# Kernel tuning notes

Measured on AMD Instinct MI355X. Metric: run time of the kernel, lower is better.

Reference implementation:

```python
import jax, jax.numpy as jnp
import numpy as np


def _lstm(x, Wx, Wh, b):
    """Fused-gate LSTM over time axis 1. x: [B,T,I]; Wx: [I,4H]; Wh: [H,4H]; b: [4H].
    Gate order (i, f, g, o) as in flax.linen.LSTMCell. Zero initial carry."""
    B, T, _ = x.shape
    H = Wh.shape[0]
    # Precompute all input-to-gate contributions in one big GEMM.
    xg = jnp.einsum('bti,ih->bth', x, Wx) + b  # [B,T,4H]

    def step(carry, xt):
        c, h = carry
        z = xt + h @ Wh  # [B,4H]
        i, f, g, o = jnp.split(z, 4, axis=-1)
        c = jax.nn.sigmoid(f) * c + jax.nn.sigmoid(i) * jnp.tanh(g)
        h = jax.nn.sigmoid(o) * jnp.tanh(c)
        return (c, h), h

    init = (jnp.zeros((B, H), x.dtype), jnp.zeros((B, H), x.dtype))
    _, hs = jax.lax.scan(step, init, jnp.swapaxes(xg, 0, 1))  # hs: [T,B,H]
    return jnp.swapaxes(hs, 0, 1)  # [B,T,H]


def _forward(X, conv_w, conv_b,
             Wx1, Wh1, b1, Wx2, Wh2, b2, Wx3, Wh3, b3, Wx4, Wh4, b4,
             Wa, ba, Va, bva, Wd1, bd1, Wd2, bd2):
    # 1-D conv, SAME padding (flax default), NWC layout.
    x = jax.lax.conv_general_dilated(X, conv_w, (1,), 'SAME',
                                     dimension_numbers=('NWC', 'WIO', 'NWC')) + conv_b
    # NOTE: source uses jnp.flip(..., axis=-1) -> flips FEATURE axis (faithful to source).
    x1 = _lstm(x, Wx1, Wh1, b1)
    x2 = _lstm(jnp.flip(x, axis=-1), Wx2, Wh2, b2)
    x = jnp.concatenate([x1, x2], axis=-1)  # [B,T,2F]
    x1 = _lstm(x, Wx3, Wh3, b3)
    x2 = _lstm(jnp.flip(x, axis=-1), Wx4, Wh4, b4)
    enc = jnp.concatenate([x1, x2], axis=-1)  # [B,T,4F]
    # Additive attention: softmax over time axis.
    score = jnp.tanh(enc @ Wa + ba) @ Va + bva  # [B,T,1]
    w = jax.nn.softmax(score, axis=1)
    ctx = jnp.sum(w * enc, axis=1)  # [B,4F]
    # MLP head (dropout deterministic -> identity).
    h = jnp.tanh(ctx @ Wd1 + bd1)
    return h @ Wd2 + bd2  # [B,1]


def setup_inputs() -> dict:
    key = jax.random.key(0)
    B, T, Cin, F = 32, 4096, 8, 64
    ks = iter(jax.random.split(key, 32))

    def w(shape):
        fan_in = shape[0] if len(shape) <= 2 else shape[0] * shape[1]
        return jax.random.normal(next(ks), shape, jnp.float32) / np.sqrt(fan_in)

    d = {}
    d['X'] = jax.random.normal(next(ks), (B, T, Cin), jnp.float32)
    d['conv_w'] = w((4, Cin, 16))
    d['conv_b'] = jnp.zeros((16,), jnp.float32)
    lstm_dims = {'1': (16, F), '2': (16, F), '3': (2 * F, 2 * F), '4': (2 * F, 2 * F)}
    for n, (i_dim, h_dim) in lstm_dims.items():
        d['Wx' + n] = w((i_dim, 4 * h_dim))
        d['Wh' + n] = w((h_dim, 4 * h_dim))
        d['b' + n] = jnp.zeros((4 * h_dim,), jnp.float32)
    d['Wa'] = w((4 * F, F)); d['ba'] = jnp.zeros((F,), jnp.float32)
    d['Va'] = w((F, 1));     d['bva'] = jnp.zeros((1,), jnp.float32)
    d['Wd1'] = w((4 * F, F)); d['bd1'] = jnp.zeros((F,), jnp.float32)
    d['Wd2'] = w((F, 1));     d['bd2'] = jnp.zeros((1,), jnp.float32)
    d['deterministic'] = 1
    return d


def reference(X, conv_w, conv_b,
              Wx1, Wh1, b1, Wx2, Wh2, b2, Wx3, Wh3, b3, Wx4, Wh4, b4,
              Wa, ba, Va, bva, Wd1, bd1, Wd2, bd2, deterministic):
    # deterministic=1 -> dropout is the identity; already reflected in _forward.
    return _forward(X, conv_w, conv_b,
                    Wx1, Wh1, b1, Wx2, Wh2, b2, Wx3, Wh3, b3, Wx4, Wh4, b4,
                    Wa, ba, Va, bva, Wd1, bd1, Wd2, bd2)
```

## Files before the change

### kernel.cpp

```cpp
#include <hip/hip_runtime.h>


#define TFULL 4096
#define NB 32

__device__ __forceinline__ float fexp2(float x){ return __builtin_amdgcn_exp2f(x); }
__device__ __forceinline__ float frcp(float x){ return __builtin_amdgcn_rcpf(x); }
__device__ __forceinline__ float sigf(float x){ return frcp(1.f + fexp2(-1.44269504f*x)); }
__device__ __forceinline__ float tanh_(float x){
    float e = fexp2(fminf(2.88539008f*x, 126.f));
    return (e - 1.f) * frcp(e + 1.f);
}
#define PIN4(v) asm volatile("" : "+v"(v.x), "+v"(v.y), "+v"(v.z), "+v"(v.w))

__global__ __launch_bounds__(256) void k_init(float* __restrict__ st1,
        float* __restrict__ st2, float* __restrict__ am, float* __restrict__ al,
        float* __restrict__ acc){
    int i = blockIdx.x * 256 + threadIdx.x;
    if (i < 8192)  st1[i] = 0.f;
    if (i < 16384) st2[i] = 0.f;
    if (i < 8192)  acc[i] = 0.f;
    if (i < 32){ am[i] = -3.4e38f; al[i] = 0.f; }
}

__global__ __launch_bounds__(256) void k_pack(
        const float* __restrict__ Wx1, const float* __restrict__ Wh1, const float* __restrict__ b1,
        const float* __restrict__ Wx2, const float* __restrict__ Wh2, const float* __restrict__ b2,
        const float* __restrict__ Wx3, const float* __restrict__ Wh3, const float* __restrict__ b3,
        const float* __restrict__ Wx4, const float* __restrict__ Wh4, const float* __restrict__ b4,
        float* __restrict__ W34, float* __restrict__ b34, float* __restrict__ W2p,
        float* __restrict__ W1p, float* __restrict__ b12){
    int i0 = blockIdx.x * 256 + threadIdx.x;
    int stride = gridDim.x * 256;
    for (int e = i0; e < 131072; e += stride){
        int k = e >> 10, n = e & 1023;
        W34[e] = (n < 512) ? Wx3[k*512 + n] : Wx4[(127 - k)*512 + (n - 512)];
    }
    for (int e = i0; e < 1024; e += stride) b34[e] = (e < 512) ? b3[e] : b4[e - 512];
    for (int e = i0; e < 131072; e += stride){
        int l = e >> 16, r = e & 65535, tid = r >> 6, widx = r & 63;
        int q = tid & 127, s = tid >> 7;
        int m = widx >> 4, kk = widx & 15;
        W2p[e] = (l ? Wh4 : Wh3)[(16*s + kk)*512 + 4*q + m];
    }
    for (int e = i0; e < 65536; e += stride){
        int l = e >> 15, r = e & 32767, tid = r >> 6, wq = r & 63;
        int q = tid & 63, s = tid >> 6;
        float v = 0.f;
        if (wq < 32){
            int c = wq >> 3, k = wq & 7;
            v = (l ? Wh2 : Wh1)[(s*8 + k)*256 + (4*q + c)];
        } else if (s < 2){
            int c = (wq - 32) >> 3, rr = (wq - 32) & 7;
            int rg = s*8 + rr, col = 4*q + c;
            v = l ? Wx2[(15 - rg)*256 + col] : Wx1[rg*256 + col];
        }
        W1p[e] = v;
    }
    for (int e = i0; e < 512; e += stride) b12[e] = (e < 256) ? b1[e] : b2[e - 256];
}

__global__ __launch_bounds__(256) void k_conv(const float* __restrict__ X,
        const float* __restrict__ W, const float* __restrict__ Bv,
        float* __restrict__ out, int t0, int lc){
    __shared__ float Ws[512];
    __shared__ float bs[16];
    int tid = threadIdx.x;
    Ws[tid] = W[tid]; Ws[tid + 256] = W[tid + 256];
    if (tid < 16) bs[tid] = Bv[tid];
    __syncthreads();
    int m = blockIdx.x * 256 + tid;
    int b = m >> lc, trel = m & ((1 << lc) - 1);
    int t = t0 + trel;
    float o[16];
    #pragma unroll
    for (int co = 0; co < 16; ++co) o[co] = bs[co];
    #pragma unroll
    for (int w = 0; w < 4; ++w){
        int tt = t + w - 1;
        if (tt >= 0 && tt < TFULL){
            const float* xr = X + ((size_t)(b << 12) + tt) * 8;
            #pragma unroll
            for (int ci = 0; ci < 8; ++ci){
                float v = xr[ci];
                #pragma unroll
                for (int co = 0; co < 16; ++co) o[co] += v * Ws[(w*8 + ci)*16 + co];
            }
        }
    }
    float* op = out + (size_t)m * 16;
    #pragma unroll
    for (int q = 0; q < 4; ++q)
        *(float4*)(op + q*4) = make_float4(o[q*4], o[q*4+1], o[q*4+2], o[q*4+3]);
}

__global__ void __launch_bounds__(512, 2)
k_scan1(const float* __restrict__ x, const float* __restrict__ W1p,
        const float* __restrict__ b12,
        float* __restrict__ cc, float* __restrict__ st1, int C){
    int l = blockIdx.x >> 5;
    int b = blockIdx.x & 31;
    int tid = threadIdx.x;
    int q = tid & 63;
    int s = tid >> 6;
    float4 w[16];
    {
        const float4* wp = (const float4*)(W1p + ((size_t)l*512 + tid)*64);
        #pragma unroll
        for (int i = 0; i < 16; ++i) w[i] = wp[i];
        #pragma unroll
        for (int i = 0; i < 16; ++i) PIN4(w[i]);
    }
    float bval = (tid < 256) ? b12[l*256 + tid] : 0.f;

    __shared__ float xs[128 * 16];
    __shared__ float zp[8 * 256];
    __shared__ float actb[256];
    __shared__ float ccbuf[128 * 64];
    __shared__ float hbufs[64];
    float c = 0.f;
    int sidx = (l*32 + b)*64 + q;
    if (tid < 64){ c = st1[sidx]; hbufs[tid] = st1[4096 + sidx]; }
    __syncthreads();

    const float* xb = x + ((size_t)b * C) * 16;
    float* ccb = cc + ((size_t)b * C) * 128 + (l << 6);
    int BS = C < 128 ? C : 128;
    int bsm = BS - 1;
    int fr = tid >> 2, fi = tid & 3;

    #pragma clang loop unroll(disable)
    for (int t = 0; t < C; ++t){
        int st = t & bsm;
        if (st == 0){
            __syncthreads();
            if (t && fr < BS){
                const float4* cb4 = (const float4*)ccbuf + fr*16 + fi*4;
                float4* cgp = (float4*)(ccb + (size_t)(t - BS + fr)*128) + fi*4;
                #pragma unroll
                for (int i = 0; i < 4; ++i) cgp[i] = cb4[i];
            }
            if (tid < BS*4)
                ((float4*)xs)[tid] = ((const float4*)(xb + (size_t)t*16))[tid];
            __syncthreads();
        }
        float a0 = 0.f, a1 = 0.f, a2 = 0.f, a3 = 0.f;
        const float4* hb4 = (const float4*)hbufs + (s << 1);
        #pragma unroll
        for (int k4 = 0; k4 < 2; ++k4){
            float4 hv = hb4[k4];
            a0 = fmaf(hv.x, w[k4].x, a0);     a0 = fmaf(hv.y, w[k4].y, a0);
            a0 = fmaf(hv.z, w[k4].z, a0);     a0 = fmaf(hv.w, w[k4].w, a0);
            a1 = fmaf(hv.x, w[2+k4].x, a1);   a1 = fmaf(hv.y, w[2+k4].y, a1);
            a1 = fmaf(hv.z, w[2+k4].z, a1);   a1 = fmaf(hv.w, w[2+k4].w, a1);
            a2 = fmaf(hv.x, w[4+k4].x, a2);   a2 = fmaf(hv.y, w[4+k4].y, a2);
            a2 = fmaf(hv.z, w[4+k4].z, a2);   a2 = fmaf(hv.w, w[4+k4].w, a2);
            a3 = fmaf(hv.x, w[6+k4].x, a3);   a3 = fmaf(hv.y, w[6+k4].y, a3);
            a3 = fmaf(hv.z, w[6+k4].z, a3);   a3 = fmaf(hv.w, w[6+k4].w, a3);
        }
        if (s < 2){
            const float4* xr = (const float4*)(xs + st * 16) + (s << 1);
            #pragma unroll
            for (int r4 = 0; r4 < 2; ++r4){
                float4 xv = xr[r4];
                a0 = fmaf(xv.x, w[8+r4].x, a0);    a0 = fmaf(xv.y, w[8+r4].y, a0);
                a0 = fmaf(xv.z, w[8+r4].z, a0);    a0 = fmaf(xv.w, w[8+r4].w, a0);
                a1 = fmaf(xv.x, w[10+r4].x, a1);   a1 = fmaf(xv.y, w[10+r4].y, a1);
                a1 = fmaf(xv.z, w[10+r4].z, a1);   a1 = fmaf(xv.w, w[10+r4].w, a1);
                a2 = fmaf(xv.x, w[12+r4].x, a2);   a2 = fmaf(xv.y, w[12+r4].y, a2);
                a2 = fmaf(xv.z, w[12+r4].z, a2);   a2 = fmaf(xv.w, w[12+r4].w, a2);
                a3 = fmaf(xv.x, w[14+r4].x, a3);   a3 = fmaf(xv.y, w[14+r4].y, a3);
                a3 = fmaf(xv.z, w[14+r4].z, a3);   a3 = fmaf(xv.w, w[14+r4].w, a3);
            }
        }
        *(float4*)(zp + (s << 8) + (q << 2)) = make_float4(a0, a1, a2, a3);
        __syncthreads();
        if (tid < 256){
            float z = bval;
            #pragma unroll
            for (int ss = 0; ss < 8; ++ss) z += zp[(ss << 8) + tid];
            actb[tid] = (tid >> 6) == 2 ? tanh_(z) : sigf(z);
        }
        __syncthreads();
        if (tid < 64){
            float gi = actb[tid], gf = actb[64 + tid];
            float gg = actb[128 + tid], go = actb[192 + tid];
            c = gf * c + gi * gg;
            float h = go * tanh_(c);
            hbufs[tid] = h;
            ccbuf[st*64 + tid] = h;
        }
        __syncthreads();
    }
    if (fr < BS){
        const float4* cb4 = (const float4*)ccbuf + fr*16 + fi*4;
        float4* cgp = (float4*)(ccb + (size_t)(C - BS + fr)*128) + fi*4;
        #pragma unroll
        for (int i = 0; i < 4; ++i) cgp[i] = cb4[i];
    }
    if (tid < 64){ st1[sidx] = c; st1[4096 + sidx] = hbufs[tid]; }
}

template<bool TANH>
__global__ __launch_bounds__(128) void k_gemm(
        const float* __restrict__ A, int lda,
        const float* __restrict__ B, int ldb,
        const float* __restrict__ bias,
        float* __restrict__ Cm, int ldc, int K){
    __shared__ float As[64 * 129];
    __shared__ float Bs[64 * 68];
    int tid = threadIdx.x;
    int tx = tid & 7;
    int ty = tid >> 3;
    int r0 = blockIdx.x * 128;
    int n0 = blockIdx.y * 64;
    float acc[8][8];
    #pragma unroll
    for (int i = 0; i < 8; ++i)
        #pragma unroll
        for (int n = 0; n < 8; ++n) acc[i][n] = 0.f;

    for (int kb = 0; kb < K; kb += 64){
        __syncthreads();
        for (int idx = tid; idx < 2048; idx += 128){
            int r = idx >> 4, k4 = idx & 15;
            float4 v = *(const float4*)(A + (size_t)(r0 + r) * lda + kb + k4*4);
            As[(k4*4 + 0)*129 + r] = v.x;
            As[(k4*4 + 1)*129 + r] = v.y;
            As[(k4*4 + 2)*129 + r] = v.z;
            As[(k4*4 + 3)*129 + r] = v.w;
        }
        for (int idx = tid; idx < 1024; idx += 128){
            int n4 = idx & 15, k = idx >> 4;
            float4 v = *(const float4*)(B + (size_t)(kb + k) * ldb + n0 + n4*4);
            *(float4*)(Bs + k*68 + n4*4) = v;
        }
        __syncthreads();
        #pragma unroll 4
        for (int k = 0; k < 64; ++k){
            float a[8];
            #pragma unroll
            for (int i = 0; i < 8; ++i) a[i] = As[k*129 + ty*8 + i];
            float4 b0 = *(const float4*)(Bs + k*68 + tx*8);
            float4 b1 = *(const float4*)(Bs + k*68 + tx*8 + 4);
            float bq[8] = {b0.x, b0.y, b0.z, b0.w, b1.x, b1.y, b1.z, b1.w};
            #pragma unroll
            for (int i = 0; i < 8; ++i)
                #pragma unroll
                for (int n = 0; n < 8; ++n) acc[i][n] += a[i] * bq[n];
        }
    }
    #pragma unroll
    for (int i = 0; i < 8; ++i){
        size_t rr = (size_t)r0 + ty*8 + i;
        float* cp = Cm + rr * ldc + n0 + tx*8;
        float ov[8];
        #pragma unroll
        for (int n = 0; n < 8; ++n){
            float v = acc[i][n] + bias[n0 + tx*8 + n];
            ov[n] = TANH ? tanh_(v) : v;
        }
        *(float4*)cp       = make_float4(ov[0], ov[1], ov[2], ov[3]);
        *(float4*)(cp + 4) = make_float4(ov[4], ov[5], ov[6], ov[7]);
    }
}

__global__ void __launch_bounds__(1024, 4)
k_scan2(const float* __restrict__ xg, const float* __restrict__ W2p,
        float* __restrict__ enc, float* __restrict__ st2, int C){
    int l = blockIdx.x >> 5;
    int b = blockIdx.x & 31;
    int tid = threadIdx.x;
    int q = tid & 127;
    int s = tid >> 7;
    float4 w[16];
    {
        const float4* wp = (const float4*)(W2p + ((size_t)l*1024 + tid)*64);
        #pragma unroll
        for (int i = 0; i < 16; ++i) w[i] = wp[i];
        #pragma unroll
        for (int i = 0; i < 16; ++i) PIN4(w[i]);
    }

    __shared__ float xgbuf[32 * 512];
    __shared__ float encbuf[32 * 128];
    __shared__ float zp[8 * 512];
    __shared__ float actb[512];
    __shared__ float hbufs[128];

    float c = 0.f;
    int sidx = (l*32 + b)*128 + q;
    if (tid < 128){ c = st2[sidx]; hbufs[tid] = st2[8192 + sidx]; }
    __syncthreads();

    const float* xgg = xg + ((size_t)b * C) * 1024 + (l << 9);
    float* encb = enc + ((size_t)b * C) * 256 + (l << 7);
    int tq = tid & 31, tr = tid >> 5;

    #pragma clang loop unroll(disable)
    for (int t = 0; t < C; ++t){
        int st = t & 31;
        if (st == 0){
            __syncthreads();
            if (t){
                float4 ev = *((const float4*)encbuf + tr*32 + tq);
                *((float4*)(encb + (size_t)(t - 32 + tr) * 256) + tq) = ev;
            }
            {
                const float4* xs4 = (const float4*)(xgg + (size_t)(t + tr) * 1024);
                float4* xb4 = (float4*)xgbuf + tr*128;
                #pragma unroll
                for (int i = 0; i < 4; ++i) xb4[tq + i*32] = xs4[tq + i*32];
            }
            __syncthreads();
        }
        float a0 = 0.f, a1 = 0.f, a2 = 0.f, a3 = 0.f;
        const float4* hb4 = (const float4*)hbufs + (s << 2);
        #pragma unroll
        for (int k4 = 0; k4 < 4; ++k4){
            float4 hv = hb4[k4];
            a0 = fmaf(hv.x, w[k4].x, a0);      a0 = fmaf(hv.y, w[k4].y, a0);
            a0 = fmaf(hv.z, w[k4].z, a0);      a0 = fmaf(hv.w, w[k4].w, a0);
            a1 = fmaf(hv.x, w[4+k4].x, a1);    a1 = fmaf(hv.y, w[4+k4].y, a1);
            a1 = fmaf(hv.z, w[4+k4].z, a1);    a1 = fmaf(hv.w, w[4+k4].w, a1);
            a2 = fmaf(hv.x, w[8+k4].x, a2);    a2 = fmaf(hv.y, w[8+k4].y, a2);
            a2 = fmaf(hv.z, w[8+k4].z, a2);    a2 = fmaf(hv.w, w[8+k4].w, a2);
            a3 = fmaf(hv.x, w[12+k4].x, a3);   a3 = fmaf(hv.y, w[12+k4].y, a3);
            a3 = fmaf(hv.z, w[12+k4].z, a3);   a3 = fmaf(hv.w, w[12+k4].w, a3);
        }
        *(float4*)(zp + (s << 9) + (q << 2)) = make_float4(a0, a1, a2, a3);
        __syncthreads();
        if (tid < 512){
            float z = xgbuf[st*512 + tid];
            #pragma unroll
            for (int ss = 0; ss < 8; ++ss) z += zp[(ss << 9) + tid];
            actb[tid] = (tid >> 7) == 2 ? tanh_(z) : sigf(z);
        }
        __syncthreads();
        if (tid < 128){
            float gi = actb[tid], gf = actb[128 + tid];
            float gg = actb[256 + tid], go = actb[384 + tid];
            c = gf * c + gi * gg;
            float h = go * tanh_(c);
            hbufs[tid] = h;
            encbuf[st*128 + tid] = h;
        }
        __syncthreads();
    }
    {
        float4 ev = *((const float4*)encbuf + tr*32 + tq);
        *((float4*)(encb + (size_t)(C - 32 + tr) * 256) + tq) = ev;
    }
    if (tid < 128){ st2[sidx] = c; st2[8192 + sidx] = hbufs[tid]; }
}

__global__ __launch_bounds__(256) void k_scorev(const float* __restrict__ u,
        const float* __restrict__ Va, const float* __restrict__ bva,
        float* __restrict__ sc){
    int m = blockIdx.x * 256 + threadIdx.x;
    const float4* up = (const float4*)(u + (size_t)m * 64);
    const float4* vp = (const float4*)Va;
    float acc = 0.f;
    #pragma unroll
    for (int i = 0; i < 16; ++i){
        float4 v = up[i], w = vp[i];
        acc += v.x*w.x + v.y*w.y + v.z*w.z + v.w*w.w;
    }
    sc[m] = acc + bva[0];
}

__global__ __launch_bounds__(1024) void k_attn(const float* __restrict__ sc,
        const float* __restrict__ enc, float* __restrict__ am,
        float* __restrict__ al, float* __restrict__ acc, int C){
    int b = blockIdx.x, tid = threadIdx.x;
    __shared__ float es[1024];
    __shared__ float red[16];
    __shared__ float sh[2];
    const float* sp = sc + (size_t)b * C;
    float mloc = -3.4e38f;
    for (int t = tid; t < C; t += 1024) mloc = fmaxf(mloc, sp[t]);
    #pragma unroll
    for (int off = 32; off; off >>= 1) mloc = fmaxf(mloc, __shfl_down(mloc, off));
    if ((tid & 63) == 0) red[tid >> 6] = mloc;
    __syncthreads();
    if (tid == 0){
        float mc = -3.4e38f;
        #pragma unroll
        for (int i = 0; i < 16; ++i) mc = fmaxf(mc, red[i]);
        float mo = am[b];
        float mn = fmaxf(mo, mc);
        sh[0] = mn;
        sh[1] = fexp2(1.44269504f * (mo - mn));
        am[b] = mn;
    }
    __syncthreads();
    float mn = sh[0], alpha = sh[1];
    float eloc = 0.f;
    for (int t = tid; t < C; t += 1024){
        float e = fexp2(1.44269504f * (sp[t] - mn));
        es[t] = e; eloc += e;
    }
    #pragma unroll
    for (int off = 32; off; off >>= 1) eloc += __shfl_down(eloc, off);
    if ((tid & 63) == 0) red[tid >> 6] = eloc;
    __syncthreads();
    if (tid == 0){
        float sm = 0.f;
        #pragma unroll
        for (int i = 0; i < 16; ++i) sm += red[i];
        al[b] = al[b] * alpha + sm;
    }
    int jf = tid & 255, sl = tid >> 8;
    int tlen = C >> 2;
    const float* ep = enc + ((size_t)b * C + (size_t)sl * tlen) * 256 + jf;
    const float* eb = es + sl * tlen;
    float a = 0.f;
    for (int t = 0; t < tlen; ++t) a = fmaf(eb[t], ep[(size_t)t * 256], a);
    __syncthreads();
    es[tid] = a;
    __syncthreads();
    if (tid < 256)
        acc[b*256 + tid] = acc[b*256 + tid] * alpha
                         + ((es[tid] + es[256 + tid]) + (es[512 + tid] + es[768 + tid]));
}

__global__ __launch_bounds__(256) void k_head(const float* __restrict__ acc,
        const float* __restrict__ al,
        const float* __restrict__ Wd1, const float* __restrict__ bd1,
        const float* __restrict__ Wd2, const float* __restrict__ bd2,
        float* __restrict__ out){
    __shared__ float ctxs[32 * 256];
    __shared__ float h1s[32 * 64];
    int tid = threadIdx.x;
    for (int idx = tid; idx < 8192; idx += 256){
        int b = idx >> 8;
        ctxs[idx] = acc[idx] / al[b];
    }
    __syncthreads();
    for (int idx = tid; idx < 2048; idx += 256){
        int b = idx >> 6, n = idx & 63;
        float a = bd1[n];
        for (int i = 0; i < 256; ++i) a += ctxs[b*256 + i] * Wd1[i*64 + n];
        h1s[idx] = tanh_(a);
    }
    __syncthreads();
    if (tid < 32){
        float a = bd2[0];
        #pragma unroll
        for (int n = 0; n < 64; ++n) a += h1s[tid*64 + n] * Wd2[n];
        out[tid] = a;
    }
}

extern "C" void kernel_launch(void* const* d_in, const int* in_sizes, int n_in,
                              void* d_out, int out_size, void* d_ws, size_t ws_size,
                              hipStream_t stream){
    const float* X     = (const float*)d_in[0];
    const float* convw = (const float*)d_in[1];
    const float* convb = (const float*)d_in[2];
    const float* Wx1 = (const float*)d_in[3];
    const float* Wh1 = (const float*)d_in[4];
    const float* b1  = (const float*)d_in[5];
    const float* Wx2 = (const float*)d_in[6];
    const float* Wh2 = (const float*)d_in[7];
    const float* b2  = (const float*)d_in[8];
    const float* Wx3 = (const float*)d_in[9];
    const float* Wh3 = (const float*)d_in[10];
    const float* b3  = (const float*)d_in[11];
    const float* Wx4 = (const float*)d_in[12];
    const float* Wh4 = (const float*)d_in[13];
    const float* b4  = (const float*)d_in[14];
    const float* Wa  = (const float*)d_in[15];
    const float* ba  = (const float*)d_in[16];
    const float* Va  = (const float*)d_in[17];
    const float* bva = (const float*)d_in[18];
    const float* Wd1 = (const float*)d_in[19];
    const float* bd1 = (const float*)d_in[20];
    const float* Wd2 = (const float*)d_in[21];
    const float* bd2 = (const float*)d_in[22];
    float* out = (float*)d_out;
    (void)in_sizes; (void)n_in; (void)out_size;

    const size_t fixedFl = 131072 + 1024 + 131072 + 65536 + 512
                         + 8192 + 16384 + 32 + 32 + 8192 + 32*1024;
    size_t capFl = ws_size / 4;
    int C = 1024;
    while (C > 32){
        size_t need = fixedFl + (size_t)NB * C * (16 + 128 + 1024 + 256 + 64);
        if (need <= capFl) break;
        C >>= 1;
    }
    int lc = 31 - __builtin_clz((unsigned)C);
    int nch = TFULL / C;

    float* ws   = (float*)d_ws;
    float* W34  = ws;
    float* b34  = W34 + 131072;
    float* W2p  = b34 + 1024;
    float* W1p  = W2p + 131072;
    float* b12  = W1p + 65536;
    float* st1  = b12 + 512;
    float* st2  = st1 + 8192;
    float* am   = st2 + 16384;
    float* al   = am + 32;
    float* acc  = al + 32;
    float* scb  = acc + 8192;
    float* xcv  = scb + 32*1024;
    float* ccb  = xcv + (size_t)NB*C*16;
    float* xgb  = ccb + (size_t)NB*C*128;
    float* enb  = xgb + (size_t)NB*C*1024;
    float* ub   = enb + (size_t)NB*C*256;

    k_init<<<64, 256, 0, stream>>>(st1, st2, am, al, acc);
    k_pack<<<512, 256, 0, stream>>>(Wx1, Wh1, b1, Wx2, Wh2, b2,
                                    Wx3, Wh3, b3, Wx4, Wh4, b4,
                                    W34, b34, W2p, W1p, b12);

    for (int ch = 0; ch < nch; ++ch){
        int t0 = ch * C;
        k_conv<<<NB*C/256, 256, 0, stream>>>(X, convw, convb, xcv, t0, lc);
        k_scan1<<<64, 512, 0, stream>>>(xcv, W1p, b12, ccb, st1, C);
        k_gemm<false><<<dim3(NB*C/128, 16), 128, 0, stream>>>(
            ccb, 128, W34, 1024, b34, xgb, 1024, 128);
        k_scan2<<<64, 1024, 0, stream>>>(xgb, W2p, enb, st2, C);
        k_gemm<true><<<dim3(NB*C/128, 1), 128, 0, stream>>>(
            enb, 256, Wa, 64, ba, ub, 64, 256);
        k_scorev<<<NB*C/256, 256, 0, stream>>>(ub, Va, bva, scb);
        k_attn<<<32, 1024, 0, stream>>>(scb, enb, am, al, acc, C);
    }
    k_head<<<1, 256, 0, stream>>>(acc, al, Wd1, bd1, Wd2, bd2, out);
}
```

Before: 5.844 ms.

## Interleave gate columns so each lane owns all four gates, dropping a barrier

Weights and biases are repacked so each thread's four partial sums map to the i,f,g,o gates of a single hidden unit rather than four adjacent columns of one gate. The per-step reduction can then compute all gate activations and the cell update in one thread, which removes the separate activation phase, the actb buffer and one __syncthreads per timestep in both recurrent scans. Scan1 also spreads the input-projection work over four slices instead of two, so fewer weight registers are needed. In exchange, activation work is concentrated in fewer threads (64 or 128) rather than spread over 256 or 512, and the launch-bounds occupancy hints are removed.

```diff
diff --git a/kernel.cpp b/kernel.cpp
--- a/kernel.cpp
+++ b/kernel.cpp
@@ -29,35 +29,41 @@
         const float* __restrict__ Wx3, const float* __restrict__ Wh3, const float* __restrict__ b3,
         const float* __restrict__ Wx4, const float* __restrict__ Wh4, const float* __restrict__ b4,
         float* __restrict__ W34, float* __restrict__ b34, float* __restrict__ W2p,
-        float* __restrict__ W1p, float* __restrict__ b12){
+        float* __restrict__ W1p, float* __restrict__ b12i){
     int i0 = blockIdx.x * 256 + threadIdx.x;
     int stride = gridDim.x * 256;
     for (int e = i0; e < 131072; e += stride){
         int k = e >> 10, n = e & 1023;
-        W34[e] = (n < 512) ? Wx3[k*512 + n] : Wx4[(127 - k)*512 + (n - 512)];
-    }
-    for (int e = i0; e < 1024; e += stride) b34[e] = (e < 512) ? b3[e] : b4[e - 512];
+        int l = n >> 9, nn = n & 511, j = nn >> 2, g = nn & 3;
+        W34[e] = l ? Wx4[(127 - k)*512 + g*128 + j] : Wx3[k*512 + g*128 + j];
+    }
+    for (int e = i0; e < 1024; e += stride){
+        int l = e >> 9, nn = e & 511, j = nn >> 2, g = nn & 3;
+        b34[e] = (l ? b4 : b3)[g*128 + j];
+    }
     for (int e = i0; e < 131072; e += stride){
         int l = e >> 16, r = e & 65535, tid = r >> 6, widx = r & 63;
         int q = tid & 127, s = tid >> 7;
         int m = widx >> 4, kk = widx & 15;
-        W2p[e] = (l ? Wh4 : Wh3)[(16*s + kk)*512 + 4*q + m];
-    }
-    for (int e = i0; e < 65536; e += stride){
-        int l = e >> 15, r = e & 32767, tid = r >> 6, wq = r & 63;
+        W2p[e] = (l ? Wh4 : Wh3)[(16*s + kk)*512 + m*128 + q];
+    }
+    for (int e = i0; e < 49152; e += stride){
+        int l = e / 24576, r = e % 24576, tid = r / 48, widx = r % 48;
         int q = tid & 63, s = tid >> 6;
+        int m = widx / 12, rem = widx % 12, k4 = rem >> 2, cmp = rem & 3;
         float v = 0.f;
-        if (wq < 32){
-            int c = wq >> 3, k = wq & 7;
-            v = (l ? Wh2 : Wh1)[(s*8 + k)*256 + (4*q + c)];
-        } else if (s < 2){
-            int c = (wq - 32) >> 3, rr = (wq - 32) & 7;
-            int rg = s*8 + rr, col = 4*q + c;
-            v = l ? Wx2[(15 - rg)*256 + col] : Wx1[rg*256 + col];
+        if (k4 < 2){
+            v = (l ? Wh2 : Wh1)[(8*s + k4*4 + cmp)*256 + m*64 + q];
+        } else if (s < 4){
+            int rr = 4*s + cmp;
+            v = l ? Wx2[(15 - rr)*256 + m*64 + q] : Wx1[rr*256 + m*64 + q];
         }
         W1p[e] = v;
     }
-    for (int e = i0; e < 512; e += stride) b12[e] = (e < 256) ? b1[e] : b2[e - 256];
+    for (int e = i0; e < 512; e += stride){
+        int l = e >> 8, nn = e & 255, j = nn >> 2, g = nn & 3;
+        b12i[e] = (l ? b2 : b1)[g*64 + j];
+    }
 }
 
 __global__ __launch_bounds__(256) void k_conv(const float* __restrict__ X,
@@ -94,28 +100,28 @@
         *(float4*)(op + q*4) = make_float4(o[q*4], o[q*4+1], o[q*4+2], o[q*4+3]);
 }
 
-__global__ void __launch_bounds__(512, 2)
+__global__ void __launch_bounds__(512)
 k_scan1(const float* __restrict__ x, const float* __restrict__ W1p,
-        const float* __restrict__ b12,
+        const float* __restrict__ b12i,
         float* __restrict__ cc, float* __restrict__ st1, int C){
     int l = blockIdx.x >> 5;
     int b = blockIdx.x & 31;
     int tid = threadIdx.x;
     int q = tid & 63;
     int s = tid >> 6;
-    float4 w[16];
+    float4 w[12];
     {
-        const float4* wp = (const float4*)(W1p + ((size_t)l*512 + tid)*64);
-        #pragma unroll
-        for (int i = 0; i < 16; ++i) w[i] = wp[i];
-        #pragma unroll
-        for (int i = 0; i < 16; ++i) PIN4(w[i]);
-    }
-    float bval = (tid < 256) ? b12[l*256 + tid] : 0.f;
+        const float4* wp = (const float4*)(W1p + ((size_t)l*512 + tid)*48);
+        #pragma unroll
+        for (int i = 0; i < 12; ++i) w[i] = wp[i];
+        #pragma unroll
+        for (int i = 0; i < 12; ++i) PIN4(w[i]);
+    }
+    float4 bi4 = make_float4(0.f, 0.f, 0.f, 0.f);
+    if (tid < 64) bi4 = *(const float4*)(b12i + l*256 + tid*4);
 
     __shared__ float xs[128 * 16];
-    __shared__ float zp[8 * 256];
-    __shared__ float actb[256];
+    __shared__ float zp1[8 * 256];
     __shared__ float ccbuf[128 * 64];
     __shared__ float hbufs[64];
     float c = 0.f;
@@ -151,40 +157,34 @@
             float4 hv = hb4[k4];
             a0 = fmaf(hv.x, w[k4].x, a0);     a0 = fmaf(hv.y, w[k4].y, a0);
             a0 = fmaf(hv.z, w[k4].z, a0);     a0 = fmaf(hv.w, w[k4].w, a0);
-            a1 = fmaf(hv.x, w[2+k4].x, a1);   a1 = fmaf(hv.y, w[2+k4].y, a1);
-            a1 = fmaf(hv.z, w[2+k4].z, a1);   a1 = fmaf(hv.w, w[2+k4].w, a1);
-            a2 = fmaf(hv.x, w[4+k4].x, a2);   a2 = fmaf(hv.y, w[4+k4].y, a2);
-            a2 = fmaf(hv.z, w[4+k4].z, a2);   a2 = fmaf(hv.w, w[4+k4].w, a2);
-            a3 = fmaf(hv.x, w[6+k4].x, a3);   a3 = fmaf(hv.y, w[6+k4].y, a3);
-            a3 = fmaf(hv.z, w[6+k4].z, a3);   a3 = fmaf(hv.w, w[6+k4].w, a3);
-        }
-        if (s < 2){
-            const float4* xr = (const float4*)(xs + st * 16) + (s << 1);
-            #pragma unroll
-            for (int r4 = 0; r4 < 2; ++r4){
-                float4 xv = xr[r4];
-                a0 = fmaf(xv.x, w[8+r4].x, a0);    a0 = fmaf(xv.y, w[8+r4].y, a0);
-                a0 = fmaf(xv.z, w[8+r4].z, a0);    a0 = fmaf(xv.w, w[8+r4].w, a0);
-                a1 = fmaf(xv.x, w[10+r4].x, a1);   a1 = fmaf(xv.y, w[10+r4].y, a1);
-                a1 = fmaf(xv.z, w[10+r4].z, a1);   a1 = fmaf(xv.w, w[10+r4].w, a1);
-                a2 = fmaf(xv.x, w[12+r4].x, a2);   a2 = fmaf(xv.y, w[12+r4].y, a2);
-                a2 = fmaf(xv.z, w[12+r4].z, a2);   a2 = fmaf(xv.w, w[12+r4].w, a2);
-                a3 = fmaf(xv.x, w[14+r4].x, a3);   a3 = fmaf(xv.y, w[14+r4].y, a3);
-                a3 = fmaf(xv.z, w[14+r4].z, a3);   a3 = fmaf(xv.w, w[14+r4].w, a3);
-            }
-        }
-        *(float4*)(zp + (s << 8) + (q << 2)) = make_float4(a0, a1, a2, a3);
-        __syncthreads();
-        if (tid < 256){
-            float z = bval;
-            #pragma unroll
-            for (int ss = 0; ss < 8; ++ss) z += zp[(ss << 8) + tid];
-            actb[tid] = (tid >> 6) == 2 ? tanh_(z) : sigf(z);
-        }
+            a1 = fmaf(hv.x, w[3+k4].x, a1);   a1 = fmaf(hv.y, w[3+k4].y, a1);
+            a1 = fmaf(hv.z, w[3+k4].z, a1);   a1 = fmaf(hv.w, w[3+k4].w, a1);
+            a2 = fmaf(hv.x, w[6+k4].x, a2);   a2 = fmaf(hv.y, w[6+k4].y, a2);
+            a2 = fmaf(hv.z, w[6+k4].z, a2);   a2 = fmaf(hv.w, w[6+k4].w, a2);
+            a3 = fmaf(hv.x, w[9+k4].x, a3);   a3 = fmaf(hv.y, w[9+k4].y, a3);
+            a3 = fmaf(hv.z, w[9+k4].z, a3);   a3 = fmaf(hv.w, w[9+k4].w, a3);
+        }
+        if (s < 4){
+            float4 xv = ((const float4*)(xs + st * 16))[s];
+            a0 = fmaf(xv.x, w[2].x, a0);    a0 = fmaf(xv.y, w[2].y, a0);
+            a0 = fmaf(xv.z, w[2].z, a0);    a0 = fmaf(xv.w, w[2].w, a0);
+            a1 = fmaf(xv.x, w[5].x, a1);    a1 = fmaf(xv.y, w[5].y, a1);
+            a1 = fmaf(xv.z, w[5].z, a1);    a1 = fmaf(xv.w, w[5].w, a1);
+            a2 = fmaf(xv.x, w[8].x, a2);    a2 = fmaf(xv.y, w[8].y, a2);
+            a2 = fmaf(xv.z, w[8].z, a2);    a2 = fmaf(xv.w, w[8].w, a2);
+            a3 = fmaf(xv.x, w[11].x, a3);   a3 = fmaf(xv.y, w[11].y, a3);
+            a3 = fmaf(xv.z, w[11].z, a3);   a3 = fmaf(xv.w, w[11].w, a3);
+        }
+        *(float4*)(zp1 + (s << 8) + (q << 2)) = make_float4(a0, a1, a2, a3);
         __syncthreads();
         if (tid < 64){
-            float gi = actb[tid], gf = actb[64 + tid];
-            float gg = actb[128 + tid], go = actb[192 + tid];
+            float4 z = bi4;
+            #pragma unroll
+            for (int ss = 0; ss < 8; ++ss){
+                float4 p = *(const float4*)(zp1 + (ss << 8) + (q << 2));
+                z.x += p.x; z.y += p.y; z.z += p.z; z.w += p.w;
+            }
+            float gi = sigf(z.x), gf = sigf(z.y), gg = tanh_(z.z), go = sigf(z.w);
             c = gf * c + gi * gg;
             float h = go * tanh_(c);
             hbufs[tid] = h;
@@ -265,7 +265,7 @@
     }
 }
 
-__global__ void __launch_bounds__(1024, 4)
+__global__ void __launch_bounds__(1024)
 k_scan2(const float* __restrict__ xg, const float* __restrict__ W2p,
         float* __restrict__ enc, float* __restrict__ st2, int C){
     int l = blockIdx.x >> 5;
@@ -283,9 +283,8 @@
     }
 
     __shared__ float xgbuf[32 * 512];
+    __shared__ float zp[8 * 512];
     __shared__ float encbuf[32 * 128];
-    __shared__ float zp[8 * 512];
-    __shared__ float actb[512];
     __shared__ float hbufs[128];
 
     float c = 0.f;
@@ -303,14 +302,14 @@
         if (st == 0){
             __syncthreads();
             if (t){
-                float4 ev = *((const float4*)encbuf + tr*32 + tq);
-                *((float4*)(encb + (size_t)(t - 32 + tr) * 256) + tq) = ev;
+                float4 ev = *(const float4*)(encbuf + tr*128 + tq*4);
+                *(float4*)(encb + (size_t)(t - 32 + tr) * 256 + tq*4) = ev;
             }
             {
-                const float4* xs4 = (const float4*)(xgg + (size_t)(t + tr) * 1024);
-                float4* xb4 = (float4*)xgbuf + tr*128;
+                const float4* src = (const float4*)(xgg + (size_t)(t + tr) * 1024);
+                float4* xb4 = (float4*)(xgbuf + tr*512);
                 #pragma unroll
-                for (int i = 0; i < 4; ++i) xb4[tq + i*32] = xs4[tq + i*32];
+                for (int i = 0; i < 4; ++i) xb4[tq + 32*i] = src[tq + 32*i];
             }
             __syncthreads();
         }
@@ -330,16 +329,14 @@
         }
         *(float4*)(zp + (s << 9) + (q << 2)) = make_float4(a0, a1, a2, a3);
         __syncthreads();
-        if (tid < 512){
-            float z = xgbuf[st*512 + tid];
+        if (tid < 128){
+            float4 z = *(const float4*)(xgbuf + (st << 9) + (q << 2));
             #pragma unroll
-            for (int ss = 0; ss < 8; ++ss) z += zp[(ss << 9) + tid];
-            actb[tid] = (tid >> 7) == 2 ? tanh_(z) : sigf(z);
-        }
-        __syncthreads();
-        if (tid < 128){
-            float gi = actb[tid], gf = actb[128 + tid];
-            float gg = actb[256 + tid], go = actb[384 + tid];
+            for (int ss = 0; ss < 8; ++ss){
+                float4 p = *(const float4*)(zp + (ss << 9) + (q << 2));
+                z.x += p.x; z.y += p.y; z.z += p.z; z.w += p.w;
+            }
+            float gi = sigf(z.x), gf = sigf(z.y), gg = tanh_(z.z), go = sigf(z.w);
             c = gf * c + gi * gg;
             float h = go * tanh_(c);
             hbufs[tid] = h;
@@ -348,8 +345,8 @@
         __syncthreads();
     }
     {
-        float4 ev = *((const float4*)encbuf + tr*32 + tq);
-        *((float4*)(encb + (size_t)(C - 32 + tr) * 256) + tq) = ev;
+        float4 ev = *(const float4*)(encbuf + tr*128 + tq*4);
+        *(float4*)(encb + (size_t)(C - 32 + tr) * 256 + tq*4) = ev;
     }
     if (tid < 128){ st2[sidx] = c; st2[8192 + sidx] = hbufs[tid]; }
 }
@@ -481,7 +478,7 @@
     float* out = (float*)d_out;
     (void)in_sizes; (void)n_in; (void)out_size;
 
-    const size_t fixedFl = 131072 + 1024 + 131072 + 65536 + 512
+    const size_t fixedFl = 131072 + 1024 + 131072 + 49152 + 512
                          + 8192 + 16384 + 32 + 32 + 8192 + 32*1024;
     size_t capFl = ws_size / 4;
     int C = 1024;
@@ -498,8 +495,8 @@
     float* b34  = W34 + 131072;
     float* W2p  = b34 + 1024;
     float* W1p  = W2p + 131072;
-    float* b12  = W1p + 65536;
-    float* st1  = b12 + 512;
+    float* b12i = W1p + 49152;
+    float* st1  = b12i + 512;
     float* st2  = st1 + 8192;
     float* am   = st2 + 16384;
     float* al   = am + 32;
@@ -514,12 +511,12 @@
     k_init<<<64, 256, 0, stream>>>(st1, st2, am, al, acc);
     k_pack<<<512, 256, 0, stream>>>(Wx1, Wh1, b1, Wx2, Wh2, b2,
                                     Wx3, Wh3, b3, Wx4, Wh4, b4,
-                                    W34, b34, W2p, W1p, b12);
+                                    W34, b34, W2p, W1p, b12i);
 
     for (int ch = 0; ch < nch; ++ch){
         int t0 = ch * C;
         k_conv<<<NB*C/256, 256, 0, stream>>>(X, convw, convb, xcv, t0, lc);
-        k_scan1<<<64, 512, 0, stream>>>(xcv, W1p, b12, ccb, st1, C);
+        k_scan1<<<64, 512, 0, stream>>>(xcv, W1p, b12i, ccb, st1, C);
         k_gemm<false><<<dim3(NB*C/128, 16), 128, 0, stream>>>(
             ccb, 128, W34, 1024, b34, xgb, 1024, 128);
         k_scan2<<<64, 1024, 0, stream>>>(xgb, W2p, enb, st2, C);
```

After: 6.011 ms. +2.8%, slower.
